# Kernel tuning notes

Hardware: AMD Instinct MI355X
Metric: run time of the kernel (lower is better)

## Reference

```python
import jax, jax.numpy as jnp
import numpy as np

B = 2048   # batch of sampled occupation configurations
L = 64     # nphysical (spatial orbitals / MPS sites)
P = 4      # local physical dimension (2 spin orbitals -> 4 occupations)
D = 128    # MPS bond dimension


def setup_inputs() -> dict:
    key = jax.random.key(0)
    k1, k2, k3, k4 = jax.random.split(key, 4)
    onstate = jax.random.randint(k1, (B, L), 0, P)  # occupation per site
    # flat MPS data buffer reshaped to [site, occupation, Dl, Dr];
    # scale by D**-0.5 so the length-L matrix chain stays O(1).
    site_tensors = jax.random.normal(k2, (L, P, D, D), dtype=jnp.float32) * (D ** -0.5)
    left_vec = jax.random.normal(k3, (D,), dtype=jnp.float32)
    right_vec = jax.random.normal(k4, (D,), dtype=jnp.float32)
    return {
        "onstate": onstate,
        "site_tensors": site_tensors,
        "left_vec": left_vec,
        "right_vec": right_vec,
    }


def reference(onstate, site_tensors, right_vec, left_vec=None, **_ignore):
    # keyword-robust shim not needed; real signature below
    raise NotImplementedError


def reference(onstate, site_tensors, left_vec, right_vec):
    """MPS amplitude: amp[b] = l^T (prod_i A[i, s_{b,i}]) r, evaluated as a
    left-to-right chain of gathered batched vector-matrix products."""
    batch = onstate.shape[0]
    s_seq = onstate.T.astype(jnp.int32)                      # [L, B]
    v0 = jnp.broadcast_to(left_vec, (batch, left_vec.shape[0]))  # [B, D]

    def step(v, inp):
        A_i, s_i = inp            # A_i: [P, D, D], s_i: [B]
        M = A_i[s_i]              # data-dependent gather -> [B, D, D]
        v = jnp.einsum('bd,bde->be', v, M)
        return v, None

    vL, _ = jax.lax.scan(step, v0, (site_tensors, s_seq))
    return vL @ right_vec         # [B] amplitudes
```

## Files before the change

### kernel.cpp

```cpp
#include <hip/hip_runtime.h>
#include <hip/hip_fp16.h>

constexpr int L = 64;
constexpr int P = 4;
constexpr int D = 128;
constexpr int B = 2048;
constexpr int EPW = 16;
constexpr int NG = B / EPW;

using v8h = __attribute__((ext_vector_type(8))) _Float16;
using v4h = __attribute__((ext_vector_type(4))) _Float16;
using v4f = __attribute__((ext_vector_type(4))) float;

constexpr size_t UT_OFF  = 0;
constexpr size_t WT_OFF  = 1048576;
constexpr size_t MTF_OFF = 2097152;
constexpr size_t MTB_OFF = 6291456;

constexpr int VLDS0 = 131072;
constexpr int VLDS1 = 131072 + 4096;
constexpr int PLDS  = 131072 + 8192;
constexpr int SMEM_BYTES = PLDS + L * EPW * 4;

#define WAIT_VM8   0xF78
#define WAIT_VM0   0xF70
#define WAIT_LGKM0 0xC07F

__device__ __forceinline__ void gl2lds16(const void* g, void* l) {
  __builtin_amdgcn_global_load_lds(
      (const __attribute__((address_space(1))) void*)g,
      (__attribute__((address_space(3))) void*)l, 16, 0, 0);
}

__global__ void convert_dual(const float* __restrict__ src,
                             _Float16* __restrict__ mtf,
                             _Float16* __restrict__ mtb) {
  __shared__ _Float16 lt[128 * 136];
  const int mat = blockIdx.x;
  const int site = mat >> 2;
  const float4* sb = (const float4*)(src + (size_t)mat * 16384);
  const int t = threadIdx.x;
  if (site >= 32) {
    _Float16* bb = mtb + (size_t)(mat - 128) * 16384;
#pragma unroll
    for (int it = 0; it < 16; ++it) {
      int idx = t + it * 256;
      float4 f = sb[idx];
      v4h h4 = {(_Float16)f.x, (_Float16)f.y, (_Float16)f.z, (_Float16)f.w};
      *(v4h*)(bb + idx * 4) = h4;
    }
    return;
  }
#pragma unroll
  for (int it = 0; it < 16; ++it) {
    int idx = t + it * 256;
    int row = idx >> 5, c4 = idx & 31;
    float4 f = sb[idx];
    lt[(c4 * 4 + 0) * 136 + row] = (_Float16)f.x;
    lt[(c4 * 4 + 1) * 136 + row] = (_Float16)f.y;
    lt[(c4 * 4 + 2) * 136 + row] = (_Float16)f.z;
    lt[(c4 * 4 + 3) * 136 + row] = (_Float16)f.w;
  }
  __syncthreads();
  _Float16* fb = mtf + (size_t)mat * 16384;
#pragma unroll
  for (int it = 0; it < 8; ++it) {
    int idx = t + it * 256;
    int c = idx >> 4, d8 = idx & 15;
    *(v8h*)(fb + c * 128 + d8 * 8) = *(const v8h*)&lt[c * 136 + d8 * 8];
  }
}

__global__ __launch_bounds__(512, 1) void mps_half_chain(
    const int* __restrict__ onstate, const _Float16* __restrict__ mtf,
    const _Float16* __restrict__ mtb, const float* __restrict__ left_vec,
    const float* __restrict__ right_vec, float* __restrict__ ut,
    float* __restrict__ wt) {
  extern __shared__ char smem[];
  const int tid = threadIdx.x;
  const int wave = tid >> 6, lane = tid & 63;
  const int me = lane & 15, q4 = lane >> 4;
  const bool fwd = !(blockIdx.x & 1);
  const int b0 = (blockIdx.x >> 1) * EPW;
  const _Float16* mbase = fwd ? mtf : mtb;
  const float* ivec = fwd ? left_vec : right_vec;
  float* ovec = fwd ? ut : wt;

  int* plds = (int*)(smem + PLDS);
#pragma unroll
  for (int j = 0; j < 2; ++j) {
    int idx = tid + j * 512;
    int e = idx >> 6, i = idx & 63;
    plds[i * EPW + e] = onstate[(b0 + e) * L + i];
  }
  if (tid < 256) {
    int e = tid >> 4, seg = tid & 15;
    _Float16* vp = (_Float16*)(smem + VLDS0) + e * 128 + (seg ^ (e & 7)) * 8;
#pragma unroll
    for (int j = 0; j < 8; ++j) vp[j] = (_Float16)ivec[seg * 8 + j];
  }

  char* wbuf = smem + wave * 16384;

  int soff[8];
#pragma unroll
  for (int i = 0; i < 8; ++i) {
    int u = i * 64 + lane;
    int p = u >> 7, r = u & 127, cl = r >> 3, slot = r & 7;
    soff[i] = p * 32768 + (wave * 16 + cl) * 256 + (slot ^ (cl & 7)) * 16;
  }
  auto stage = [&](int ls, int h, int z) {
    const char* gb = (const char*)mbase + (size_t)ls * 131072 + h * 128;
    char* lb = wbuf + z * 8192;
#pragma unroll
    for (int i = 0; i < 8; ++i) gl2lds16(gb + soff[i], lb + i * 1024);
  };
  auto consume = [&](int h, int z, int pm, const char* vb, v4f& acc) {
    const int s0 = h * 8 + q4, s1 = h * 8 + 4 + q4;
    v8h a0 = *(const v8h*)(vb + me * 256 + (s0 ^ (me & 7)) * 16);
    v8h a1 = *(const v8h*)(vb + me * 256 + (s1 ^ (me & 7)) * 16);
    const char* cb = wbuf + z * 8192;
#pragma unroll
    for (int p = 0; p < P; ++p) {
      const bool isp = (pm == p);
      v8h zf = {};
      v8h am0 = isp ? a0 : zf;
      v8h am1 = isp ? a1 : zf;
      const char* pb = cb + p * 2048 + me * 128;
      v8h bf0 = *(const v8h*)(pb + ((q4) ^ (me & 7)) * 16);
      v8h bf1 = *(const v8h*)(pb + ((4 + q4) ^ (me & 7)) * 16);
      acc = __builtin_amdgcn_mfma_f32_16x16x32_f16(am0, bf0, acc, 0, 0, 0);
      acc = __builtin_amdgcn_mfma_f32_16x16x32_f16(am1, bf1, acc, 0, 0, 0);
    }
  };

  stage(fwd ? 0 : 31, 0, 0);
  __syncthreads();

  const int c0 = wave * 16 + me;
  v4f accL = {0.f, 0.f, 0.f, 0.f};
  for (int site = 0; site < 32; ++site) {
    const int site_g = fwd ? site : 63 - site;
    const int ls     = fwd ? site : 31 - site;
    const int pm = plds[site_g * EPW + me];
    const char* vb = smem + ((site & 1) ? VLDS1 : VLDS0);
    v4f acc = {0.f, 0.f, 0.f, 0.f};

    stage(ls, 1, 1);
    consume(0, 0, pm, vb, acc);

    if (site < 31) {
      const int lsn = fwd ? site + 1 : 30 - site;
      __builtin_amdgcn_sched_barrier(0);
      __builtin_amdgcn_s_waitcnt(WAIT_LGKM0);
      __builtin_amdgcn_sched_barrier(0);
      stage(lsn, 0, 0);
      __builtin_amdgcn_s_waitcnt(WAIT_VM8);
      consume(1, 1, pm, vb, acc);
      _Float16* vn = (_Float16*)(smem + ((site & 1) ? VLDS0 : VLDS1));
#pragma unroll
      for (int r = 0; r < 4; ++r) {
        int e = q4 * 4 + r;
        vn[e * 128 + ((c0 >> 3) ^ (e & 7)) * 8 + (c0 & 7)] = (_Float16)acc[r];
      }
      __syncthreads();
    } else {
      __builtin_amdgcn_s_waitcnt(WAIT_VM0);
      consume(1, 1, pm, vb, acc);
      accL = acc;
    }
  }
#pragma unroll
  for (int r = 0; r < 4; ++r) ovec[c0 * B + b0 + q4 * 4 + r] = accL[r];
}

__global__ void combine_uw(const float* __restrict__ ut,
                           const float* __restrict__ wt,
                           float* __restrict__ out) {
  const int b = blockIdx.x * 256 + threadIdx.x;
  float s = 0.f;
#pragma unroll 8
  for (int d = 0; d < D; ++d) s += ut[d * B + b] * wt[d * B + b];
  out[b] = s;
}

extern "C" void kernel_launch(void* const* d_in, const int* in_sizes, int n_in,
                              void* d_out, int out_size, void* d_ws,
                              size_t ws_size, hipStream_t stream) {
  const int*   onstate      = (const int*)d_in[0];
  const float* site_tensors = (const float*)d_in[1];
  const float* left_vec     = (const float*)d_in[2];
  const float* right_vec    = (const float*)d_in[3];
  float*       out          = (float*)d_out;
  char*        ws           = (char*)d_ws;
  float*       ut           = (float*)(ws + UT_OFF);
  float*       wt           = (float*)(ws + WT_OFF);
  _Float16*    mtf          = (_Float16*)(ws + MTF_OFF);
  _Float16*    mtb          = (_Float16*)(ws + MTB_OFF);

  hipFuncSetAttribute((const void*)mps_half_chain,
                      hipFuncAttributeMaxDynamicSharedMemorySize, SMEM_BYTES);

  convert_dual<<<L * P, 256, 0, stream>>>(site_tensors, mtf, mtb);
  mps_half_chain<<<2 * NG, 512, SMEM_BYTES, stream>>>(
      onstate, mtf, mtb, left_vec, right_vec, ut, wt);
  combine_uw<<<B / 256, 256, 0, stream>>>(ut, wt, out);
}
```

Before: 134.5 us.

## Load site matrices directly into registers with double buffering instead of LDS staging

Replaces the global-to-LDS async staging of each site's fp16 matrix slices with direct global loads into register arrays, double-buffered across sites (the next site is prefetched while the current one is consumed by MFMA). This shrinks LDS to the small vector and occupation buffers and drops the dynamic shared-memory setup. It also swaps __syncthreads for an explicit lgkm wait plus s_barrier. The cost is high register pressure from holding 32 v8h fragments per lane, and global load latency now depends on the compiler scheduling rather than explicit vmcnt waits.

```diff
diff --git a/kernel.cpp b/kernel.cpp
--- a/kernel.cpp
+++ b/kernel.cpp
@@ -17,20 +17,7 @@
 constexpr size_t MTF_OFF = 2097152;
 constexpr size_t MTB_OFF = 6291456;
 
-constexpr int VLDS0 = 131072;
-constexpr int VLDS1 = 131072 + 4096;
-constexpr int PLDS  = 131072 + 8192;
-constexpr int SMEM_BYTES = PLDS + L * EPW * 4;
-
-#define WAIT_VM8   0xF78
-#define WAIT_VM0   0xF70
 #define WAIT_LGKM0 0xC07F
-
-__device__ __forceinline__ void gl2lds16(const void* g, void* l) {
-  __builtin_amdgcn_global_load_lds(
-      (const __attribute__((address_space(1))) void*)g,
-      (__attribute__((address_space(3))) void*)l, 16, 0, 0);
-}
 
 __global__ void convert_dual(const float* __restrict__ src,
                              _Float16* __restrict__ mtf,
@@ -71,12 +58,13 @@
   }
 }
 
-__global__ __launch_bounds__(512, 1) void mps_half_chain(
+__global__ __launch_bounds__(512, 1) void mps_half_chain2(
     const int* __restrict__ onstate, const _Float16* __restrict__ mtf,
     const _Float16* __restrict__ mtb, const float* __restrict__ left_vec,
     const float* __restrict__ right_vec, float* __restrict__ ut,
     float* __restrict__ wt) {
-  extern __shared__ char smem[];
+  __shared__ _Float16 vlds[2][EPW * D];
+  __shared__ int plds[L * EPW];
   const int tid = threadIdx.x;
   const int wave = tid >> 6, lane = tid & 63;
   const int me = lane & 15, q4 = lane >> 4;
@@ -86,7 +74,6 @@
   const float* ivec = fwd ? left_vec : right_vec;
   float* ovec = fwd ? ut : wt;
 
-  int* plds = (int*)(smem + PLDS);
 #pragma unroll
   for (int j = 0; j < 2; ++j) {
     int idx = tid + j * 512;
@@ -95,81 +82,76 @@
   }
   if (tid < 256) {
     int e = tid >> 4, seg = tid & 15;
-    _Float16* vp = (_Float16*)(smem + VLDS0) + e * 128 + (seg ^ (e & 7)) * 8;
+    _Float16* vp = &vlds[0][e * 128 + (seg ^ (e & 7)) * 8];
 #pragma unroll
     for (int j = 0; j < 8; ++j) vp[j] = (_Float16)ivec[seg * 8 + j];
   }
 
-  char* wbuf = smem + wave * 16384;
+  const char* lb = (const char*)mbase + (wave * 16 + me) * 256 + q4 * 16;
+  const int c0 = wave * 16 + me;
 
-  int soff[8];
+  auto loadsite = [&](int ls, v8h (&dst)[2][8]) {
+    const char* sbase = lb + (size_t)ls * 131072;
 #pragma unroll
-  for (int i = 0; i < 8; ++i) {
-    int u = i * 64 + lane;
-    int p = u >> 7, r = u & 127, cl = r >> 3, slot = r & 7;
-    soff[i] = p * 32768 + (wave * 16 + cl) * 256 + (slot ^ (cl & 7)) * 16;
-  }
-  auto stage = [&](int ls, int h, int z) {
-    const char* gb = (const char*)mbase + (size_t)ls * 131072 + h * 128;
-    char* lb = wbuf + z * 8192;
+    for (int h = 0; h < 2; ++h)
 #pragma unroll
-    for (int i = 0; i < 8; ++i) gl2lds16(gb + soff[i], lb + i * 1024);
+      for (int p = 0; p < P; ++p)
+#pragma unroll
+        for (int kc = 0; kc < 2; ++kc)
+          dst[h][p * 2 + kc] =
+              *(const v8h*)(sbase + p * 32768 + h * 128 + kc * 64);
   };
-  auto consume = [&](int h, int z, int pm, const char* vb, v4f& acc) {
+  auto consume = [&](const v8h (&bb)[8], int h, int pm, const char* vb,
+                     v4f& acc) {
     const int s0 = h * 8 + q4, s1 = h * 8 + 4 + q4;
     v8h a0 = *(const v8h*)(vb + me * 256 + (s0 ^ (me & 7)) * 16);
     v8h a1 = *(const v8h*)(vb + me * 256 + (s1 ^ (me & 7)) * 16);
-    const char* cb = wbuf + z * 8192;
 #pragma unroll
     for (int p = 0; p < P; ++p) {
       const bool isp = (pm == p);
       v8h zf = {};
       v8h am0 = isp ? a0 : zf;
       v8h am1 = isp ? a1 : zf;
-      const char* pb = cb + p * 2048 + me * 128;
-      v8h bf0 = *(const v8h*)(pb + ((q4) ^ (me & 7)) * 16);
-      v8h bf1 = *(const v8h*)(pb + ((4 + q4) ^ (me & 7)) * 16);
-      acc = __builtin_amdgcn_mfma_f32_16x16x32_f16(am0, bf0, acc, 0, 0, 0);
-      acc = __builtin_amdgcn_mfma_f32_16x16x32_f16(am1, bf1, acc, 0, 0, 0);
+      acc = __builtin_amdgcn_mfma_f32_16x16x32_f16(am0, bb[p * 2 + 0], acc,
+                                                   0, 0, 0);
+      acc = __builtin_amdgcn_mfma_f32_16x16x32_f16(am1, bb[p * 2 + 1], acc,
+                                                   0, 0, 0);
     }
   };
 
-  stage(fwd ? 0 : 31, 0, 0);
+  v8h bufA[2][8], bufB[2][8];
+  loadsite(fwd ? 0 : 31, bufA);
   __syncthreads();
 
-  const int c0 = wave * 16 + me;
   v4f accL = {0.f, 0.f, 0.f, 0.f};
-  for (int site = 0; site < 32; ++site) {
+  auto step = [&](int site, v8h (&cur)[2][8], v8h (&nxt)[2][8]) {
     const int site_g = fwd ? site : 63 - site;
-    const int ls     = fwd ? site : 31 - site;
     const int pm = plds[site_g * EPW + me];
-    const char* vb = smem + ((site & 1) ? VLDS1 : VLDS0);
+    const char* vb = (const char*)vlds[site & 1];
+    if (site < 31) loadsite(fwd ? site + 1 : 30 - site, nxt);
     v4f acc = {0.f, 0.f, 0.f, 0.f};
-
-    stage(ls, 1, 1);
-    consume(0, 0, pm, vb, acc);
-
+    consume(cur[0], 0, pm, vb, acc);
+    consume(cur[1], 1, pm, vb, acc);
     if (site < 31) {
-      const int lsn = fwd ? site + 1 : 30 - site;
-      __builtin_amdgcn_sched_barrier(0);
-      __builtin_amdgcn_s_waitcnt(WAIT_LGKM0);
-      __builtin_amdgcn_sched_barrier(0);
-      stage(lsn, 0, 0);
-      __builtin_amdgcn_s_waitcnt(WAIT_VM8);
-      consume(1, 1, pm, vb, acc);
-      _Float16* vn = (_Float16*)(smem + ((site & 1) ? VLDS0 : VLDS1));
+      _Float16* vn = (_Float16*)vlds[(site & 1) ^ 1];
 #pragma unroll
       for (int r = 0; r < 4; ++r) {
         int e = q4 * 4 + r;
         vn[e * 128 + ((c0 >> 3) ^ (e & 7)) * 8 + (c0 & 7)] = (_Float16)acc[r];
       }
-      __syncthreads();
+      __builtin_amdgcn_s_waitcnt(WAIT_LGKM0);
+      __builtin_amdgcn_s_barrier();
     } else {
-      __builtin_amdgcn_s_waitcnt(WAIT_VM0);
-      consume(1, 1, pm, vb, acc);
       accL = acc;
     }
+  };
+
+#pragma unroll 1
+  for (int s2 = 0; s2 < 16; ++s2) {
+    step(2 * s2 + 0, bufA, bufB);
+    step(2 * s2 + 1, bufB, bufA);
   }
+
 #pragma unroll
   for (int r = 0; r < 4; ++r) ovec[c0 * B + b0 + q4 * 4 + r] = accL[r];
 }
@@ -198,11 +180,8 @@
   _Float16*    mtf          = (_Float16*)(ws + MTF_OFF);
   _Float16*    mtb          = (_Float16*)(ws + MTB_OFF);
 
-  hipFuncSetAttribute((const void*)mps_half_chain,
-                      hipFuncAttributeMaxDynamicSharedMemorySize, SMEM_BYTES);
-
   convert_dual<<<L * P, 256, 0, stream>>>(site_tensors, mtf, mtb);
-  mps_half_chain<<<2 * NG, 512, SMEM_BYTES, stream>>>(
+  mps_half_chain2<<<2 * NG, 512, 0, stream>>>(
       onstate, mtf, mtb, left_vec, right_vec, ut, wt);
   combine_uw<<<B / 256, 256, 0, stream>>>(ut, wt, out);
 }
```

Result: slower. 203.3 us (+51.1%).
